# Kernel optimization log

Measured on AMD Instinct MI355X. Metric: run time of the kernel, lower is better.

Reference implementation:

```python
import jax, jax.numpy as jnp
import numpy as np

UNITS = 256
NUM_HEADS = 8
HEAD_DIM = UNITS // NUM_HEADS
B, N = 8, 2048


def setup_inputs() -> dict:
    key = jax.random.key(0)
    ks = jax.random.split(key, 7)
    node_features = jax.random.normal(ks[0], (B, N, UNITS), dtype=jnp.float32)
    adjacency_matrix = jax.random.randint(ks[1], (B, N, N), 0, 2, dtype=jnp.int32)
    # Glorot-ish scaled dense weights
    s = 1.0 / np.sqrt(UNITS)
    Wq = jax.random.normal(ks[2], (UNITS, UNITS), dtype=jnp.float32) * s
    Wk = jax.random.normal(ks[3], (UNITS, UNITS), dtype=jnp.float32) * s
    Wv = jax.random.normal(ks[4], (UNITS, UNITS), dtype=jnp.float32) * s
    Wo = jax.random.normal(ks[5], (UNITS, UNITS), dtype=jnp.float32) * s
    bo = jnp.zeros((UNITS,), dtype=jnp.float32)
    return {"node_features": node_features, "adjacency_matrix": adjacency_matrix,
            "Wq": Wq, "Wk": Wk, "Wv": Wv, "Wo": Wo, "bo": bo}


def reference(node_features, adjacency_matrix, Wq, Wk, Wv, Wo, bo):
    b, n, _ = node_features.shape
    h, d = NUM_HEADS, HEAD_DIM
    # projections -> [b, h, n, d]
    q = (node_features @ Wq).reshape(b, n, h, d).transpose(0, 2, 1, 3)
    k = (node_features @ Wk).reshape(b, n, h, d).transpose(0, 2, 1, 3)
    v = (node_features @ Wv).reshape(b, n, h, d).transpose(0, 2, 1, 3)
    scores = jnp.einsum('bhqd,bhkd->bhqk', q, k) / jnp.sqrt(jnp.float32(d))
    mask = adjacency_matrix[:, None, :, :] > 0  # [b,1,n,n] broadcasts over heads
    scores = jnp.where(mask, scores, jnp.float32(-1e9))
    w = jax.nn.softmax(scores, axis=-1)
    # dropout is identity at inference (training=None)
    ctx = jnp.einsum('bhqk,bhkd->bhqd', w, v)
    ctx = ctx.transpose(0, 2, 1, 3).reshape(b, n, h * d)
    return ctx @ Wo + bo
```

## Files before the change

kernel.cpp:

```cpp
#include <hip/hip_runtime.h>
#include <cstdint>
#include <cstddef>

#define B_ 8
#define N_ 2048
#define H_ 8
#define D_ 32
#define U_ 256

typedef _Float16 half8 __attribute__((ext_vector_type(8)));
typedef _Float16 half4 __attribute__((ext_vector_type(4)));
typedef float float4v __attribute__((ext_vector_type(4)));

__device__ __forceinline__ float fast_exp2(float x) {
#if __has_builtin(__builtin_amdgcn_exp2f)
  return __builtin_amdgcn_exp2f(x);
#else
  return exp2f(x);
#endif
}

__global__ __launch_bounds__(256)
void k_prep(const float* __restrict__ X,
            const float* __restrict__ Wq, const float* __restrict__ Wk,
            const float* __restrict__ Wv, const float* __restrict__ Wo,
            _Float16* __restrict__ Xh, _Float16* __restrict__ WT)
{
  __shared__ __attribute__((aligned(16))) float Ts[64][68];
  const int tid = threadIdx.x;
  const int bx = blockIdx.x;
  if (bx < 64) {
    const int wsel = bx >> 4;
    const int t    = bx & 15;
    const float* W = (wsel == 0) ? Wq : (wsel == 1) ? Wk : (wsel == 2) ? Wv : Wo;
    const float scale = (wsel == 0) ? 0.25505413f : 1.0f;
    _Float16* dstW = WT + (size_t)wsel * (U_ * U_);
    const int r = tid >> 2, cs = tid & 3;
    const int k0 = (t >> 2) * 64, n0 = (t & 3) * 64;
#pragma unroll
    for (int j = 0; j < 4; ++j)
      *(float4v*)&Ts[r][cs * 16 + j * 4] =
          *(const float4v*)(W + (size_t)(k0 + r) * U_ + n0 + cs * 16 + j * 4);
    __syncthreads();
#pragma unroll
    for (int j = 0; j < 4; ++j) {
      half4 hv;
#pragma unroll
      for (int jj = 0; jj < 4; ++jj)
        hv[jj] = (_Float16)(Ts[cs * 16 + j * 4 + jj][r] * scale);
      *(half4*)(dstW + (size_t)(n0 + r) * U_ + k0 + cs * 16 + j * 4) = hv;
    }
  } else {
    const size_t base = ((size_t)(bx - 64) * 256 + tid) * 32;
#pragma unroll
    for (int i = 0; i < 4; ++i) {
      float4v a  = *(const float4v*)(X + base + i * 8);
      float4v b2 = *(const float4v*)(X + base + i * 8 + 4);
      half8 hv;
      hv[0] = (_Float16)a[0];  hv[1] = (_Float16)a[1];
      hv[2] = (_Float16)a[2];  hv[3] = (_Float16)a[3];
      hv[4] = (_Float16)b2[0]; hv[5] = (_Float16)b2[1];
      hv[6] = (_Float16)b2[2]; hv[7] = (_Float16)b2[3];
      *(half8*)(Xh + base + i * 8) = hv;
    }
  }
}

__global__ __launch_bounds__(256, 2)
void k_qkv2(const _Float16* __restrict__ Xh,
            const _Float16* __restrict__ WTq, const _Float16* __restrict__ WTk,
            const _Float16* __restrict__ WTv,
            _Float16* __restrict__ Qg, _Float16* __restrict__ Kg,
            _Float16* __restrict__ VTg)
{
  __shared__ __attribute__((aligned(16))) char qsmem[27648];
  _Float16* Xs = (_Float16*)qsmem;
  _Float16* Ws = (_Float16*)(qsmem + 9216);

  const int tid  = threadIdx.x;
  const int lane = tid & 63;
  const int w    = tid >> 6;
  const int c    = lane & 15;
  const int qd   = lane >> 4;

  const int bx   = blockIdx.x;
  const int proj = bx >> 1;
  const int nh   = bx & 1;
  const int n0l  = nh * 128;
  const int m0   = blockIdx.y * 64;
  const _Float16* WT = (proj == 0) ? WTq : ((proj == 1) ? WTk : WTv);

  const float4v zero4 = {0.f, 0.f, 0.f, 0.f};
  float4v acc[8];
#pragma unroll
  for (int j = 0; j < 8; ++j) acc[j] = zero4;

  const int xrow = tid >> 2, xoff = (tid & 3) * 16;
  const int wrow = tid >> 1, woff = (tid & 1) * 32;
  for (int kt = 0; kt < 4; ++kt) {
    const int k0 = kt * 64;
    {
      const _Float16* src = Xh + (size_t)(m0 + xrow) * U_ + k0 + xoff;
      _Float16* dst = &Xs[xrow * 72 + xoff];
      *(half8*)(dst)     = *(const half8*)(src);
      *(half8*)(dst + 8) = *(const half8*)(src + 8);
    }
    {
      const _Float16* srcw = WT + (size_t)(n0l + wrow) * U_ + k0 + woff;
      _Float16* dstw = &Ws[wrow * 72 + woff];
#pragma unroll
      for (int i = 0; i < 4; ++i)
        *(half8*)(dstw + i * 8) = *(const half8*)(srcw + i * 8);
    }
    __syncthreads();
#pragma unroll
    for (int ks = 0; ks < 2; ++ks) {
      half8 af = *(const half8*)&Xs[(w * 16 + c) * 72 + ks * 32 + qd * 8];
      half8 bf[8];
#pragma unroll
      for (int nt = 0; nt < 8; ++nt)
        bf[nt] = *(const half8*)&Ws[(nt * 16 + c) * 72 + ks * 32 + qd * 8];
#pragma unroll
      for (int nt = 0; nt < 8; ++nt)
        acc[nt] = __builtin_amdgcn_mfma_f32_16x16x32_f16(af, bf[nt], acc[nt], 0, 0, 0);
    }
    __syncthreads();
  }

  const int b   = m0 >> 11;
  const int nb0 = m0 & (N_ - 1);
  if (proj < 2) {
    _Float16* Og = (proj == 0) ? Qg : Kg;
#pragma unroll
    for (int nt = 0; nt < 8; ++nt)
#pragma unroll
      for (int r = 0; r < 4; ++r) {
        const int rowl = w * 16 + qd * 4 + r;
        Og[(size_t)(b * N_ + nb0 + rowl) * U_ + n0l + nt * 16 + c] = (_Float16)acc[nt][r];
      }
  } else {
    _Float16* tr = (_Float16*)qsmem;
#pragma unroll
    for (int nt = 0; nt < 8; ++nt)
#pragma unroll
      for (int r = 0; r < 4; ++r)
        tr[(nt * 16 + c) * 72 + w * 16 + qd * 4 + r] = (_Float16)acc[nt][r];
    __syncthreads();
    const int u = tid >> 1;
    const int seg = tid & 1;
    _Float16* dst = VTg + (size_t)(b * U_ + n0l + u) * N_ + nb0 + seg * 32;
#pragma unroll
    for (int i = 0; i < 4; ++i)
      *(half8*)(dst + i * 8) = *(const half8*)&tr[u * 72 + seg * 32 + i * 8];
  }
}

__global__ __launch_bounds__(256, 2)
void k_qkv(const float* __restrict__ X,
           const float* __restrict__ Wq, const float* __restrict__ Wk,
           const float* __restrict__ Wv,
           _Float16* __restrict__ Qg, _Float16* __restrict__ Kg,
           _Float16* __restrict__ VTg)
{
  __shared__ __attribute__((aligned(16))) char qsmem[36864];
  _Float16* Xs = (_Float16*)qsmem;
  _Float16* Ws = (_Float16*)(qsmem + 18432);

  const int tid  = threadIdx.x;
  const int lane = tid & 63;
  const int w    = tid >> 6;
  const int c    = lane & 15;
  const int qd   = lane >> 4;

  const int bx   = blockIdx.x;
  const int proj = bx >> 1;
  const int nh   = bx & 1;
  const int n0l  = nh * 128;
  const int m0   = blockIdx.y * 128;
  const float* Wp = (proj == 0) ? Wq : ((proj == 1) ? Wk : Wv);
  const float wscale = (proj == 0) ? 0.25505413f : 1.0f;

  const float4v zero4 = {0.f, 0.f, 0.f, 0.f};
  float4v acc[2][8];
#pragma unroll
  for (int i = 0; i < 2; ++i)
#pragma unroll
    for (int j = 0; j < 8; ++j) acc[i][j] = zero4;

  for (int kt = 0; kt < 4; ++kt) {
    const int k0 = kt * 64;
    {
      const int row = tid >> 1;
      const int off = (tid & 1) * 32;
      const float* src = X + (size_t)(m0 + row) * U_ + k0 + off;
      _Float16* dst = &Xs[row * 72 + off];
#pragma unroll
      for (int i = 0; i < 4; ++i) {
        float4v a  = *(const float4v*)(src + i * 8);
        float4v b2 = *(const float4v*)(src + i * 8 + 4);
        half8 hv;
        hv[0] = (_Float16)a[0];  hv[1] = (_Float16)a[1];
        hv[2] = (_Float16)a[2];  hv[3] = (_Float16)a[3];
        hv[4] = (_Float16)b2[0]; hv[5] = (_Float16)b2[1];
        hv[6] = (_Float16)b2[2]; hv[7] = (_Float16)b2[3];
        *(half8*)(dst + i * 8) = hv;
      }
    }
    {
      const int kl = tid & 63;
      const int ng = tid >> 6;
      const float* srcw = Wp + (size_t)(k0 + kl) * U_ + n0l + ng * 32;
#pragma unroll
      for (int j = 0; j < 8; ++j) {
        float4v a = *(const float4v*)(srcw + j * 4);
#pragma unroll
        for (int jj = 0; jj < 4; ++jj)
          Ws[(ng * 32 + j * 4 + jj) * 72 + kl] = (_Float16)(a[jj] * wscale);
      }
    }
    __syncthreads();
#pragma unroll
    for (int ks = 0; ks < 2; ++ks) {
      half8 af[2], bf[8];
#pragma unroll
      for (int mt = 0; mt < 2; ++mt)
        af[mt] = *(const half8*)&Xs[(w * 32 + mt * 16 + c) * 72 + ks * 32 + qd * 8];
#pragma unroll
      for (int nt = 0; nt < 8; ++nt)
        bf[nt] = *(const half8*)&Ws[(nt * 16 + c) * 72 + ks * 32 + qd * 8];
#pragma unroll
      for (int mt = 0; mt < 2; ++mt)
#pragma unroll
        for (int nt = 0; nt < 8; ++nt)
          acc[mt][nt] = __builtin_amdgcn_mfma_f32_16x16x32_f16(af[mt], bf[nt], acc[mt][nt], 0, 0, 0);
    }
    __syncthreads();
  }

  const int b   = m0 >> 11;
  const int nb0 = m0 & (N_ - 1);
  if (proj < 2) {
    _Float16* Og = (proj == 0) ? Qg : Kg;
#pragma unroll
    for (int mt = 0; mt < 2; ++mt)
#pragma unroll
      for (int nt = 0; nt < 8; ++nt)
#pragma unroll
        for (int r = 0; r < 4; ++r) {
          const int rowl = w * 32 + mt * 16 + qd * 4 + r;
          Og[(size_t)(b * N_ + nb0 + rowl) * U_ + n0l + nt * 16 + c] = (_Float16)acc[mt][nt][r];
        }
  } else {
    _Float16* tr = (_Float16*)qsmem;
#pragma unroll
    for (int mt = 0; mt < 2; ++mt)
#pragma unroll
      for (int nt = 0; nt < 8; ++nt)
#pragma unroll
        for (int r = 0; r < 4; ++r)
          tr[(nt * 16 + c) * 136 + w * 32 + mt * 16 + qd * 4 + r] = (_Float16)acc[mt][nt][r];
    __syncthreads();
    const int u = tid >> 1;
    const int seg = tid & 1;
    _Float16* dst = VTg + (size_t)(b * U_ + n0l + u) * N_ + nb0 + seg * 64;
#pragma unroll
    for (int i = 0; i < 8; ++i)
      *(half8*)(dst + i * 8) = *(const half8*)&tr[u * 136 + seg * 64 + i * 8];
  }
}

#define KS_H (32 * 264)
#define VT_H (256 * 40)

struct StageRegs {
  half8 k0, v0;
  int a0, a1;
};

__global__ __launch_bounds__(1024, 4)
void k_attn(const _Float16* __restrict__ Qg, const _Float16* __restrict__ Kg,
            const _Float16* __restrict__ VTg, const int* __restrict__ Adj,
            const _Float16* __restrict__ WTo, const float* __restrict__ bo,
            float* __restrict__ Out)
{
  __shared__ __attribute__((aligned(16))) _Float16 KsB[2][KS_H];
  __shared__ __attribute__((aligned(16))) _Float16 VTsB[2][VT_H];
  __shared__ __attribute__((aligned(8)))  unsigned int maskB[2][64];

  const int tid  = threadIdx.x;
  const int lane = tid & 63;
  const int w    = tid >> 6;
  const int h    = w & 7;
  const int qh   = w >> 3;
  const int c    = lane & 15;
  const int qd   = lane >> 4;
  const int wg   = blockIdx.x;
  const int b    = wg & 7;
  const int q0   = (wg >> 3) * 64;

  const _Float16* kptr = Kg + (size_t)(b * N_ + (tid >> 5)) * U_ + (tid & 31) * 8;
  const _Float16* vptr = VTg + (size_t)(b * U_ + (tid >> 2)) * N_ + (tid & 3) * 8;
  const int rr = lane >> 5;
  const int kk = lane & 31;
  const int* aptr = Adj + (size_t)(b * N_ + q0 + w * 4 + rr) * N_ + kk;

  half8 qb[2];
#pragma unroll
  for (int nt = 0; nt < 2; ++nt)
    qb[nt] = *(const half8*)(Qg + (size_t)(b * N_ + q0 + qh * 32 + nt * 16 + c) * U_ + h * D_ + qd * 8);

  const float4v init4 = {-8.f, -8.f, -8.f, -8.f};
  const float4v zero4 = {0.f, 0.f, 0.f, 0.f};
  float4v acc[2][2];
#pragma unroll
  for (int i = 0; i < 2; ++i)
#pragma unroll
    for (int j = 0; j < 2; ++j) acc[i][j] = zero4;
  float lrow[2] = {0.f, 0.f};

  auto load_tile = [&](int kt) -> StageRegs {
    StageRegs r;
    r.k0 = *(const half8*)(kptr + (size_t)kt * 32 * U_);
    r.v0 = *(const half8*)(vptr + (size_t)kt * 32);
    const int* as = aptr + (size_t)kt * 32;
    r.a0 = as[0];
    r.a1 = as[2 * N_];
    return r;
  };
  auto store_tile = [&](const StageRegs& r, int buf) {
    *(half8*)&KsB[buf][(tid >> 5) * 264 + (tid & 31) * 8] = r.k0;
    *(half8*)&VTsB[buf][(tid >> 2) * 40 + (tid & 3) * 8] = r.v0;
    unsigned long long bm;
    bm = __ballot(r.a0 > 0); if (lane == 0) *(unsigned long long*)&maskB[buf][w * 4 + 0] = bm;
    bm = __ballot(r.a1 > 0); if (lane == 0) *(unsigned long long*)&maskB[buf][w * 4 + 2] = bm;
  };
  auto compute_tile = [&](int buf) {
    half8 ka0 = *(const half8*)&KsB[buf][(0 * 16 + c) * 264 + h * D_ + qd * 8];
    half8 ka1 = *(const half8*)&KsB[buf][(1 * 16 + c) * 264 + h * D_ + qd * 8];
    half4 va[2][2];
#pragma unroll
    for (int mt = 0; mt < 2; ++mt)
#pragma unroll
      for (int kc = 0; kc < 2; ++kc)
        va[mt][kc] = *(const half4*)&VTsB[buf][(h * D_ + mt * 16 + c) * 40 + kc * 16 + qd * 4];
#pragma unroll
    for (int nt = 0; nt < 2; ++nt) {
      float4v s0 = __builtin_amdgcn_mfma_f32_16x16x32_f16(ka0, qb[nt], init4, 0, 0, 0);
      float4v s1 = __builtin_amdgcn_mfma_f32_16x16x32_f16(ka1, qb[nt], init4, 0, 0, 0);
      const unsigned int mq = maskB[buf][qh * 32 + nt * 16 + c];
      const unsigned int t0 = mq >> (qd * 4);
      const unsigned int t1 = mq >> (16 + qd * 4);
      half4 pb0, pb1;
      float ls = 0.f;
#pragma unroll
      for (int r = 0; r < 4; ++r) {
        float e0 = fast_exp2(s0[r]);
        float e1 = fast_exp2(s1[r]);
        float p0 = ((t0 >> r) & 1u) ? e0 : 0.f;
        float p1 = ((t1 >> r) & 1u) ? e1 : 0.f;
        ls += p0 + p1;
        pb0[r] = (_Float16)p0;
        pb1[r] = (_Float16)p1;
      }
      lrow[nt] += ls;
      acc[0][nt] = __builtin_amdgcn_mfma_f32_16x16x16f16(va[0][0], pb0, acc[0][nt], 0, 0, 0);
      acc[0][nt] = __builtin_amdgcn_mfma_f32_16x16x16f16(va[0][1], pb1, acc[0][nt], 0, 0, 0);
      acc[1][nt] = __builtin_amdgcn_mfma_f32_16x16x16f16(va[1][0], pb0, acc[1][nt], 0, 0, 0);
      acc[1][nt] = __builtin_amdgcn_mfma_f32_16x16x16f16(va[1][1], pb1, acc[1][nt], 0, 0, 0);
    }
  };

  StageRegs rA = load_tile(0);
  store_tile(rA, 0);
  StageRegs rB = load_tile(1);
  __syncthreads();

#pragma unroll 1
  for (int kt = 0; kt < 64; kt += 2) {
    if (kt + 2 < 64) rA = load_tile(kt + 2);
    compute_tile(0);
    store_tile(rB, 1);
    __syncthreads();
    if (kt + 3 < 64) rB = load_tile(kt + 3);
    compute_tile(1);
    if (kt + 2 < 64) store_tile(rA, 0);
    __syncthreads();
  }

  float rinv[2];
#pragma unroll
  for (int nt = 0; nt < 2; ++nt) {
    float l = lrow[nt];
    l += __shfl_xor(l, 16, 64);
    l += __shfl_xor(l, 32, 64);
    rinv[nt] = (l > 0.f) ? 1.f / l : 0.f;
  }
  _Float16* ctxS = (_Float16*)KsB;
#pragma unroll
  for (int mt = 0; mt < 2; ++mt)
#pragma unroll
    for (int nt = 0; nt < 2; ++nt) {
      half4 hv;
#pragma unroll
      for (int r = 0; r < 4; ++r)
        hv[r] = (_Float16)(acc[mt][nt][r] * rinv[nt]);
      *(half4*)&ctxS[(qh * 32 + nt * 16 + c) * 264 + h * D_ + mt * 16 + qd * 4] = hv;
    }
  __syncthreads();

  const int n0w = w * 16;
  float4v oacc[4] = {zero4, zero4, zero4, zero4};
#pragma unroll
  for (int ks = 0; ks < 8; ++ks) {
    half8 bf = *(const half8*)(WTo + (size_t)(n0w + c) * U_ + ks * 32 + qd * 8);
#pragma unroll
    for (int mt = 0; mt < 4; ++mt) {
      half8 af = *(const half8*)&ctxS[(mt * 16 + c) * 264 + ks * 32 + qd * 8];
      oacc[mt] = __builtin_amdgcn_mfma_f32_16x16x32_f16(af, bf, oacc[mt], 0, 0, 0);
    }
  }
  const float bias = bo[n0w + c];
#pragma unroll
  for (int mt = 0; mt < 4; ++mt)
#pragma unroll
    for (int r = 0; r < 4; ++r) {
      const int rowl = mt * 16 + qd * 4 + r;
      Out[(size_t)(b * N_ + q0 + rowl) * U_ + n0w + c] = oacc[mt][r] + bias;
    }
}

extern "C" void kernel_launch(void* const* d_in, const int* in_sizes, int n_in,
                              void* d_out, int out_size, void* d_ws, size_t ws_size,
                              hipStream_t stream) {
  const float* X   = (const float*)d_in[0];
  const int*   Adj = (const int*)d_in[1];
  const float* Wq  = (const float*)d_in[2];
  const float* Wk  = (const float*)d_in[3];
  const float* Wv  = (const float*)d_in[4];
  const float* Wo  = (const float*)d_in[5];
  const float* bo  = (const float*)d_in[6];
  float* Out = (float*)d_out;

  const size_t elems = (size_t)B_ * N_ * U_;
  const size_t wsz   = (size_t)U_ * U_;
  const size_t need_full = (4 * elems + 4 * wsz) * sizeof(_Float16);

  if (ws_size >= need_full) {
    _Float16* Xh  = (_Float16*)d_ws;
    _Float16* Qg  = Xh + elems;
    _Float16* Kg  = Qg + elems;
    _Float16* VTg = Kg + elems;
    _Float16* WT  = VTg + elems;
    _Float16* WTq = WT;
    _Float16* WTk = WT + wsz;
    _Float16* WTv = WT + 2 * wsz;
    _Float16* WTo = WT + 3 * wsz;

    k_prep<<<dim3(64 + 512), 256, 0, stream>>>(X, Wq, Wk, Wv, Wo, Xh, WT);
    k_qkv2<<<dim3(6, 256), 256, 0, stream>>>(Xh, WTq, WTk, WTv, Qg, Kg, VTg);
    k_attn<<<dim3(256), 1024, 0, stream>>>(Qg, Kg, VTg, Adj, WTo, bo, Out);
  } else {
    _Float16* Qg  = (_Float16*)d_ws;
    _Float16* Kg  = Qg + elems;
    _Float16* VTg = Kg + elems;
    _Float16* WT  = VTg + elems;
    _Float16* WTo = WT + 3 * wsz;

    k_prep<<<dim3(64), 256, 0, stream>>>(X, Wq, Wk, Wv, Wo, Qg , WT);
    k_qkv<<<dim3(6, 128), 256, 0, stream>>>(X, Wq, Wk, Wv, Qg, Kg, VTg);
    k_attn<<<dim3(256), 1024, 0, stream>>>(Qg, Kg, VTg, Adj, WTo, bo, Out);
  }
}
```

Baseline: 303.7 us.

## Fuse X fp16 conversion into QKV projection with register-resident weight fragments

Drops the separate X-to-fp16 pass in the prep kernel and its round trip through workspace. The new QKV kernel converts a 64x256 X tile straight into shared memory and holds each wave's weight B-fragments in registers for the full K loop, so the k-tiled loop and its per-tile syncs go away. Each 64-row X tile is now converted six times (once per projection half-block), and the larger register footprint and 33KB of LDS per block may limit occupancy. The fallback path for small workspaces is removed.

```diff
diff --git a/kernel.cpp b/kernel.cpp
--- a/kernel.cpp
+++ b/kernel.cpp
@@ -21,130 +21,120 @@
 }
 
 __global__ __launch_bounds__(256)
-void k_prep(const float* __restrict__ X,
-            const float* __restrict__ Wq, const float* __restrict__ Wk,
+void k_prep(const float* __restrict__ Wq, const float* __restrict__ Wk,
             const float* __restrict__ Wv, const float* __restrict__ Wo,
-            _Float16* __restrict__ Xh, _Float16* __restrict__ WT)
+            _Float16* __restrict__ WT)
 {
   __shared__ __attribute__((aligned(16))) float Ts[64][68];
   const int tid = threadIdx.x;
   const int bx = blockIdx.x;
-  if (bx < 64) {
-    const int wsel = bx >> 4;
-    const int t    = bx & 15;
-    const float* W = (wsel == 0) ? Wq : (wsel == 1) ? Wk : (wsel == 2) ? Wv : Wo;
-    const float scale = (wsel == 0) ? 0.25505413f : 1.0f;
-    _Float16* dstW = WT + (size_t)wsel * (U_ * U_);
-    const int r = tid >> 2, cs = tid & 3;
-    const int k0 = (t >> 2) * 64, n0 = (t & 3) * 64;
-#pragma unroll
-    for (int j = 0; j < 4; ++j)
-      *(float4v*)&Ts[r][cs * 16 + j * 4] =
-          *(const float4v*)(W + (size_t)(k0 + r) * U_ + n0 + cs * 16 + j * 4);
-    __syncthreads();
-#pragma unroll
-    for (int j = 0; j < 4; ++j) {
-      half4 hv;
-#pragma unroll
-      for (int jj = 0; jj < 4; ++jj)
-        hv[jj] = (_Float16)(Ts[cs * 16 + j * 4 + jj][r] * scale);
-      *(half4*)(dstW + (size_t)(n0 + r) * U_ + k0 + cs * 16 + j * 4) = hv;
-    }
-  } else {
-    const size_t base = ((size_t)(bx - 64) * 256 + tid) * 32;
-#pragma unroll
-    for (int i = 0; i < 4; ++i) {
-      float4v a  = *(const float4v*)(X + base + i * 8);
-      float4v b2 = *(const float4v*)(X + base + i * 8 + 4);
+  const int wsel = bx >> 4;
+  const int t    = bx & 15;
+  const float* W = (wsel == 0) ? Wq : (wsel == 1) ? Wk : (wsel == 2) ? Wv : Wo;
+  const float scale = (wsel == 0) ? 0.25505413f : 1.0f;
+  _Float16* dstW = WT + (size_t)wsel * (U_ * U_);
+  const int r = tid >> 2, cs = tid & 3;
+  const int k0 = (t >> 2) * 64, n0 = (t & 3) * 64;
+#pragma unroll
+  for (int j = 0; j < 4; ++j)
+    *(float4v*)&Ts[r][cs * 16 + j * 4] =
+        *(const float4v*)(W + (size_t)(k0 + r) * U_ + n0 + cs * 16 + j * 4);
+  __syncthreads();
+#pragma unroll
+  for (int j = 0; j < 4; ++j) {
+    half4 hv;
+#pragma unroll
+    for (int jj = 0; jj < 4; ++jj)
+      hv[jj] = (_Float16)(Ts[cs * 16 + j * 4 + jj][r] * scale);
+    *(half4*)(dstW + (size_t)(n0 + r) * U_ + k0 + cs * 16 + j * 4) = hv;
+  }
+}
+
+__global__ __launch_bounds__(256)
+void k_qkv3(const float* __restrict__ X, const _Float16* __restrict__ WT,
+            _Float16* __restrict__ Qg, _Float16* __restrict__ Kg,
+            _Float16* __restrict__ VTg)
+{
+  __shared__ __attribute__((aligned(16))) _Float16 Xs[64 * 264];
+
+  const int tid  = threadIdx.x;
+  const int lane = tid & 63;
+  const int w    = tid >> 6;
+  const int c    = lane & 15;
+  const int qd   = lane >> 4;
+
+  const int bx   = blockIdx.x;
+  const int proj = bx >> 1;
+  const int nh   = bx & 1;
+  const int n0l  = nh * 128;
+  const int m0   = blockIdx.y * 64;
+  const _Float16* WTp = WT + (size_t)proj * (U_ * U_);
+
+  half8 bf[2][8];
+#pragma unroll
+  for (int nt = 0; nt < 2; ++nt)
+#pragma unroll
+    for (int ks = 0; ks < 8; ++ks)
+      bf[nt][ks] = *(const half8*)(WTp + (size_t)(n0l + w * 32 + nt * 16 + c) * U_ + ks * 32 + qd * 8);
+
+  {
+    const int row  = tid >> 2;
+    const int col0 = (tid & 3) * 64;
+    const float* src = X + (size_t)(m0 + row) * U_ + col0;
+    _Float16* dst = &Xs[row * 264 + col0];
+#pragma unroll
+    for (int i = 0; i < 8; ++i) {
+      float4v a  = *(const float4v*)(src + i * 8);
+      float4v b2 = *(const float4v*)(src + i * 8 + 4);
       half8 hv;
       hv[0] = (_Float16)a[0];  hv[1] = (_Float16)a[1];
       hv[2] = (_Float16)a[2];  hv[3] = (_Float16)a[3];
       hv[4] = (_Float16)b2[0]; hv[5] = (_Float16)b2[1];
       hv[6] = (_Float16)b2[2]; hv[7] = (_Float16)b2[3];
-      *(half8*)(Xh + base + i * 8) = hv;
-    }
-  }
-}
-
-__global__ __launch_bounds__(256, 2)
-void k_qkv2(const _Float16* __restrict__ Xh,
-            const _Float16* __restrict__ WTq, const _Float16* __restrict__ WTk,
-            const _Float16* __restrict__ WTv,
-            _Float16* __restrict__ Qg, _Float16* __restrict__ Kg,
-            _Float16* __restrict__ VTg)
-{
-  __shared__ __attribute__((aligned(16))) char qsmem[27648];
-  _Float16* Xs = (_Float16*)qsmem;
-  _Float16* Ws = (_Float16*)(qsmem + 9216);
-
-  const int tid  = threadIdx.x;
-  const int lane = tid & 63;
-  const int w    = tid >> 6;
-  const int c    = lane & 15;
-  const int qd   = lane >> 4;
-
-  const int bx   = blockIdx.x;
-  const int proj = bx >> 1;
-  const int nh   = bx & 1;
-  const int n0l  = nh * 128;
-  const int m0   = blockIdx.y * 64;
-  const _Float16* WT = (proj == 0) ? WTq : ((proj == 1) ? WTk : WTv);
+      *(half8*)(dst + i * 8) = hv;
+    }
+  }
+  __syncthreads();
 
   const float4v zero4 = {0.f, 0.f, 0.f, 0.f};
-  float4v acc[8];
-#pragma unroll
-  for (int j = 0; j < 8; ++j) acc[j] = zero4;
-
-  const int xrow = tid >> 2, xoff = (tid & 3) * 16;
-  const int wrow = tid >> 1, woff = (tid & 1) * 32;
-  for (int kt = 0; kt < 4; ++kt) {
-    const int k0 = kt * 64;
-    {
-      const _Float16* src = Xh + (size_t)(m0 + xrow) * U_ + k0 + xoff;
-      _Float16* dst = &Xs[xrow * 72 + xoff];
-      *(half8*)(dst)     = *(const half8*)(src);
-      *(half8*)(dst + 8) = *(const half8*)(src + 8);
-    }
-    {
-      const _Float16* srcw = WT + (size_t)(n0l + wrow) * U_ + k0 + woff;
-      _Float16* dstw = &Ws[wrow * 72 + woff];
-#pragma unroll
-      for (int i = 0; i < 4; ++i)
-        *(half8*)(dstw + i * 8) = *(const half8*)(srcw + i * 8);
-    }
-    __syncthreads();
-#pragma unroll
-    for (int ks = 0; ks < 2; ++ks) {
-      half8 af = *(const half8*)&Xs[(w * 16 + c) * 72 + ks * 32 + qd * 8];
-      half8 bf[8];
-#pragma unroll
-      for (int nt = 0; nt < 8; ++nt)
-        bf[nt] = *(const half8*)&Ws[(nt * 16 + c) * 72 + ks * 32 + qd * 8];
-#pragma unroll
-      for (int nt = 0; nt < 8; ++nt)
-        acc[nt] = __builtin_amdgcn_mfma_f32_16x16x32_f16(af, bf[nt], acc[nt], 0, 0, 0);
-    }
-    __syncthreads();
-  }
+  float4v acc[4][2];
+#pragma unroll
+  for (int i = 0; i < 4; ++i)
+#pragma unroll
+    for (int j = 0; j < 2; ++j) acc[i][j] = zero4;
+
+#pragma unroll
+  for (int ks = 0; ks < 8; ++ks)
+#pragma unroll
+    for (int mf = 0; mf < 4; ++mf) {
+      half8 af = *(const half8*)&Xs[(mf * 16 + c) * 264 + ks * 32 + qd * 8];
+      acc[mf][0] = __builtin_amdgcn_mfma_f32_16x16x32_f16(af, bf[0][ks], acc[mf][0], 0, 0, 0);
+      acc[mf][1] = __builtin_amdgcn_mfma_f32_16x16x32_f16(af, bf[1][ks], acc[mf][1], 0, 0, 0);
+    }
 
   const int b   = m0 >> 11;
   const int nb0 = m0 & (N_ - 1);
   if (proj < 2) {
     _Float16* Og = (proj == 0) ? Qg : Kg;
 #pragma unroll
-    for (int nt = 0; nt < 8; ++nt)
-#pragma unroll
-      for (int r = 0; r < 4; ++r) {
-        const int rowl = w * 16 + qd * 4 + r;
-        Og[(size_t)(b * N_ + nb0 + rowl) * U_ + n0l + nt * 16 + c] = (_Float16)acc[nt][r];
-      }
+    for (int mf = 0; mf < 4; ++mf)
+#pragma unroll
+      for (int nt = 0; nt < 2; ++nt)
+#pragma unroll
+        for (int r = 0; r < 4; ++r) {
+          const int rowl = mf * 16 + qd * 4 + r;
+          Og[(size_t)(b * N_ + nb0 + rowl) * U_ + n0l + w * 32 + nt * 16 + c] = (_Float16)acc[mf][nt][r];
+        }
   } else {
-    _Float16* tr = (_Float16*)qsmem;
-#pragma unroll
-    for (int nt = 0; nt < 8; ++nt)
-#pragma unroll
-      for (int r = 0; r < 4; ++r)
-        tr[(nt * 16 + c) * 72 + w * 16 + qd * 4 + r] = (_Float16)acc[nt][r];
+    __syncthreads();
+    _Float16* tr = Xs;
+#pragma unroll
+    for (int mf = 0; mf < 4; ++mf)
+#pragma unroll
+      for (int nt = 0; nt < 2; ++nt)
+#pragma unroll
+        for (int r = 0; r < 4; ++r)
+          tr[(w * 32 + nt * 16 + c) * 72 + mf * 16 + qd * 4 + r] = (_Float16)acc[mf][nt][r];
     __syncthreads();
     const int u = tid >> 1;
     const int seg = tid & 1;
@@ -152,120 +142,6 @@
 #pragma unroll
     for (int i = 0; i < 4; ++i)
       *(half8*)(dst + i * 8) = *(const half8*)&tr[u * 72 + seg * 32 + i * 8];
-  }
-}
-
-__global__ __launch_bounds__(256, 2)
-void k_qkv(const float* __restrict__ X,
-           const float* __restrict__ Wq, const float* __restrict__ Wk,
-           const float* __restrict__ Wv,
-           _Float16* __restrict__ Qg, _Float16* __restrict__ Kg,
-           _Float16* __restrict__ VTg)
-{
-  __shared__ __attribute__((aligned(16))) char qsmem[36864];
-  _Float16* Xs = (_Float16*)qsmem;
-  _Float16* Ws = (_Float16*)(qsmem + 18432);
-
-  const int tid  = threadIdx.x;
-  const int lane = tid & 63;
-  const int w    = tid >> 6;
-  const int c    = lane & 15;
-  const int qd   = lane >> 4;
-
-  const int bx   = blockIdx.x;
-  const int proj = bx >> 1;
-  const int nh   = bx & 1;
-  const int n0l  = nh * 128;
-  const int m0   = blockIdx.y * 128;
-  const float* Wp = (proj == 0) ? Wq : ((proj == 1) ? Wk : Wv);
-  const float wscale = (proj == 0) ? 0.25505413f : 1.0f;
-
-  const float4v zero4 = {0.f, 0.f, 0.f, 0.f};
-  float4v acc[2][8];
-#pragma unroll
-  for (int i = 0; i < 2; ++i)
-#pragma unroll
-    for (int j = 0; j < 8; ++j) acc[i][j] = zero4;
-
-  for (int kt = 0; kt < 4; ++kt) {
-    const int k0 = kt * 64;
-    {
-      const int row = tid >> 1;
-      const int off = (tid & 1) * 32;
-      const float* src = X + (size_t)(m0 + row) * U_ + k0 + off;
-      _Float16* dst = &Xs[row * 72 + off];
-#pragma unroll
-      for (int i = 0; i < 4; ++i) {
-        float4v a  = *(const float4v*)(src + i * 8);
-        float4v b2 = *(const float4v*)(src + i * 8 + 4);
-        half8 hv;
-        hv[0] = (_Float16)a[0];  hv[1] = (_Float16)a[1];
-        hv[2] = (_Float16)a[2];  hv[3] = (_Float16)a[3];
-        hv[4] = (_Float16)b2[0]; hv[5] = (_Float16)b2[1];
-        hv[6] = (_Float16)b2[2]; hv[7] = (_Float16)b2[3];
-        *(half8*)(dst + i * 8) = hv;
-      }
-    }
-    {
-      const int kl = tid & 63;
-      const int ng = tid >> 6;
-      const float* srcw = Wp + (size_t)(k0 + kl) * U_ + n0l + ng * 32;
-#pragma unroll
-      for (int j = 0; j < 8; ++j) {
-        float4v a = *(const float4v*)(srcw + j * 4);
-#pragma unroll
-        for (int jj = 0; jj < 4; ++jj)
-          Ws[(ng * 32 + j * 4 + jj) * 72 + kl] = (_Float16)(a[jj] * wscale);
-      }
-    }
-    __syncthreads();
-#pragma unroll
-    for (int ks = 0; ks < 2; ++ks) {
-      half8 af[2], bf[8];
-#pragma unroll
-      for (int mt = 0; mt < 2; ++mt)
-        af[mt] = *(const half8*)&Xs[(w * 32 + mt * 16 + c) * 72 + ks * 32 + qd * 8];
-#pragma unroll
-      for (int nt = 0; nt < 8; ++nt)
-        bf[nt] = *(const half8*)&Ws[(nt * 16 + c) * 72 + ks * 32 + qd * 8];
-#pragma unroll
-      for (int mt = 0; mt < 2; ++mt)
-#pragma unroll
-        for (int nt = 0; nt < 8; ++nt)
-          acc[mt][nt] = __builtin_amdgcn_mfma_f32_16x16x32_f16(af[mt], bf[nt], acc[mt][nt], 0, 0, 0);
-    }
-    __syncthreads();
-  }
-
-  const int b   = m0 >> 11;
-  const int nb0 = m0 & (N_ - 1);
-  if (proj < 2) {
-    _Float16* Og = (proj == 0) ? Qg : Kg;
-#pragma unroll
-    for (int mt = 0; mt < 2; ++mt)
-#pragma unroll
-      for (int nt = 0; nt < 8; ++nt)
-#pragma unroll
-        for (int r = 0; r < 4; ++r) {
-          const int rowl = w * 32 + mt * 16 + qd * 4 + r;
-          Og[(size_t)(b * N_ + nb0 + rowl) * U_ + n0l + nt * 16 + c] = (_Float16)acc[mt][nt][r];
-        }
-  } else {
-    _Float16* tr = (_Float16*)qsmem;
-#pragma unroll
-    for (int mt = 0; mt < 2; ++mt)
-#pragma unroll
-      for (int nt = 0; nt < 8; ++nt)
-#pragma unroll
-        for (int r = 0; r < 4; ++r)
-          tr[(nt * 16 + c) * 136 + w * 32 + mt * 16 + qd * 4 + r] = (_Float16)acc[mt][nt][r];
-    __syncthreads();
-    const int u = tid >> 1;
-    const int seg = tid & 1;
-    _Float16* dst = VTg + (size_t)(b * U_ + n0l + u) * N_ + nb0 + seg * 64;
-#pragma unroll
-    for (int i = 0; i < 8; ++i)
-      *(half8*)(dst + i * 8) = *(const half8*)&tr[u * 136 + seg * 64 + i * 8];
   }
 }
 
@@ -443,31 +319,14 @@
 
   const size_t elems = (size_t)B_ * N_ * U_;
   const size_t wsz   = (size_t)U_ * U_;
-  const size_t need_full = (4 * elems + 4 * wsz) * sizeof(_Float16);
-
-  if (ws_size >= need_full) {
-    _Float16* Xh  = (_Float16*)d_ws;
-    _Float16* Qg  = Xh + elems;
-    _Float16* Kg  = Qg + elems;
-    _Float16* VTg = Kg + elems;
-    _Float16* WT  = VTg + elems;
-    _Float16* WTq = WT;
-    _Float16* WTk = WT + wsz;
-    _Float16* WTv = WT + 2 * wsz;
-    _Float16* WTo = WT + 3 * wsz;
-
-    k_prep<<<dim3(64 + 512), 256, 0, stream>>>(X, Wq, Wk, Wv, Wo, Xh, WT);
-    k_qkv2<<<dim3(6, 256), 256, 0, stream>>>(Xh, WTq, WTk, WTv, Qg, Kg, VTg);
-    k_attn<<<dim3(256), 1024, 0, stream>>>(Qg, Kg, VTg, Adj, WTo, bo, Out);
-  } else {
-    _Float16* Qg  = (_Float16*)d_ws;
-    _Float16* Kg  = Qg + elems;
-    _Float16* VTg = Kg + elems;
-    _Float16* WT  = VTg + elems;
-    _Float16* WTo = WT + 3 * wsz;
-
-    k_prep<<<dim3(64), 256, 0, stream>>>(X, Wq, Wk, Wv, Wo, Qg , WT);
-    k_qkv<<<dim3(6, 128), 256, 0, stream>>>(X, Wq, Wk, Wv, Qg, Kg, VTg);
-    k_attn<<<dim3(256), 1024, 0, stream>>>(Qg, Kg, VTg, Adj, WTo, bo, Out);
-  }
-}
+
+  _Float16* Qg  = (_Float16*)d_ws;
+  _Float16* Kg  = Qg + elems;
+  _Float16* VTg = Kg + elems;
+  _Float16* WT  = VTg + elems;
+  _Float16* WTo = WT + 3 * wsz;
+
+  k_prep<<<dim3(64), 256, 0, stream>>>(Wq, Wk, Wv, Wo, WT);
+  k_qkv3<<<dim3(6, 256), 256, 0, stream>>>(X, WT, Qg, Kg, VTg);
+  k_attn<<<dim3(256), 1024, 0, stream>>>(Qg, Kg, VTg, Adj, WTo, bo, Out);
+}
```

New measurement: 310.9 us. +2.4%, slower.
